# Kernel tuning notes

Hardware: AMD Instinct MI355X
Metric: run time of the kernel (lower is better)

Reference implementation:

```python
import jax, jax.numpy as jnp
import numpy as np

EPS = 1e-5

def rmsnorm(x, g):
    var = jnp.mean(jnp.square(x), axis=-1, keepdims=True)
    return x * jax.lax.rsqrt(var + EPS) * g

def setup_inputs() -> dict:
    key = jax.random.key(0)
    ks = jax.random.split(key, 8)
    B, S, T, D = 2, 2048, 2048, 1024
    H, HKV, HD = 16, 4, 64
    std = 0.02
    return {
        "x": jax.random.normal(ks[0], (B, S, D), jnp.float32),
        "kv": jax.random.normal(ks[1], (B, T, D), jnp.float32),
        "wq": jax.random.normal(ks[2], (H * HD, D), jnp.float32) * std,
        "wk": jax.random.normal(ks[3], (HKV * HD, D), jnp.float32) * std,
        "wv": jax.random.normal(ks[4], (HKV * HD, D), jnp.float32) * std,
        "wo": jax.random.normal(ks[5], (D, H * HD), jnp.float32) * std,
        "gq": jnp.ones((D,), jnp.float32),
        "gkv": jnp.ones((D,), jnp.float32),
    }

def reference(x, kv, wq, wk, wv, wo, gq, gkv):
    B, S, D = x.shape
    T = kv.shape[1]
    H, HKV, HD = 16, 4, 64
    R = H // HKV  # heads per kv group
    xn = rmsnorm(x, gq)
    kvn = rmsnorm(kv, gkv)
    # projections
    q = (xn @ wq.T).reshape(B, S, HKV, R, HD)   # grouped query heads
    k = (kvn @ wk.T).reshape(B, T, HKV, HD)
    v = (kvn @ wv.T).reshape(B, T, HKV, HD)
    scale = 1.0 / jnp.sqrt(jnp.float32(HD))
    # block-mask is None -> full dense cross attention; GQA via broadcast einsum
    scores = jnp.einsum('bsgrd,btgd->bgrst', q, k) * scale  # [B,HKV,R,S,T]
    probs = jax.nn.softmax(scores, axis=-1)
    out = jnp.einsum('bgrst,btgd->bsgrd', probs, v)  # [B,S,HKV,R,HD]
    out = out.reshape(B, S, H * HD) @ wo.T
    return x + out
```

## Files before the change

### kernel.cpp

```cpp
#include <hip/hip_runtime.h>

#define DEV __device__ __forceinline__

typedef __attribute__((ext_vector_type(8))) short frag8;
typedef __attribute__((ext_vector_type(8))) _Float16 h8;
typedef __attribute__((ext_vector_type(4))) float f32x4;

DEV unsigned short f2bf(float f) {
  union { float f; unsigned int u; } v; v.f = f;
  unsigned int r = v.u + 0x7fffu + ((v.u >> 16) & 1u);
  return (unsigned short)(r >> 16);
}

DEV unsigned short f2h(float f) {
  union { _Float16 h[2]; unsigned short u[2]; } v;
  v.h[0] = (_Float16)f;
  return v.u[0];
}

DEV float h2f(unsigned short u) {
  union { _Float16 h[2]; unsigned short u[2]; } v;
  v.u[0] = u;
  return (float)v.h[0];
}

DEV unsigned int pack2h(float a, float b) {
  union { __fp16 __attribute__((ext_vector_type(2))) p; unsigned int u; } v;
  v.p = __builtin_amdgcn_cvt_pkrtz(a, b);
  return v.u;
}

DEV void async_load16(const void* g, void* l) {
  __builtin_amdgcn_global_load_lds(
      (const __attribute__((address_space(1))) void*)g,
      (__attribute__((address_space(3))) void*)l,
      16, 0, 0);
}

__global__ __launch_bounds__(256) void fused_cast(const float* __restrict__ wq,
                                                  const float* __restrict__ wk,
                                                  const float* __restrict__ wv,
                                                  const float* __restrict__ wo,
                                                  unsigned short* __restrict__ wqb,
                                                  unsigned short* __restrict__ wkvb,
                                                  unsigned short* __restrict__ wob,
                                                  float qscale) {
  const int b = blockIdx.x;
  const float* src;
  unsigned short* dst;
  float sc = 1.0f;
  int base;
  if (b < 1024) { src = wq; dst = wqb; sc = qscale; base = b; }
  else if (b < 1280) { src = wk; dst = wkvb; base = b - 1024; }
  else if (b < 1536) { src = wv; dst = wkvb + 262144; base = b - 1280; }
  else { src = wo; dst = wob; base = b - 1536; }
  const int i = (base * 256 + threadIdx.x) * 4;
  float4 v = *(const float4*)&src[i];
  ushort4 o;
  o.x = f2bf(v.x * sc); o.y = f2bf(v.y * sc);
  o.z = f2bf(v.z * sc); o.w = f2bf(v.w * sc);
  *(ushort4*)&dst[i] = o;
}

__global__ __launch_bounds__(256) void rmsnorm2(const float* __restrict__ x,
                                                const float* __restrict__ kv,
                                                const float* __restrict__ gq,
                                                const float* __restrict__ gkv,
                                                unsigned short* __restrict__ xn,
                                                unsigned short* __restrict__ kvn) {
  int row = blockIdx.x;
  const int tid = threadIdx.x;
  const float* src;
  const float* g;
  unsigned short* dst;
  if (row < 4096) { src = x; g = gq; dst = xn; }
  else { row -= 4096; src = kv; g = gkv; dst = kvn; }
  const float* xr = src + (size_t)row * 1024;
  float4 v = *(const float4*)&xr[tid * 4];
  float ss = v.x * v.x + v.y * v.y + v.z * v.z + v.w * v.w;
  ss += __shfl_xor(ss, 32); ss += __shfl_xor(ss, 16);
  ss += __shfl_xor(ss, 8);  ss += __shfl_xor(ss, 4);
  ss += __shfl_xor(ss, 2);  ss += __shfl_xor(ss, 1);
  __shared__ float red[4];
  if ((tid & 63) == 0) red[tid >> 6] = ss;
  __syncthreads();
  float tot = red[0] + red[1] + red[2] + red[3];
  float inv = rsqrtf(tot * (1.0f / 1024.0f) + 1e-5f);
  float4 gv = *(const float4*)&g[tid * 4];
  ushort4 o;
  o.x = f2bf(v.x * inv * gv.x); o.y = f2bf(v.y * inv * gv.y);
  o.z = f2bf(v.z * inv * gv.z); o.w = f2bf(v.w * inv * gv.w);
  *(ushort4*)&dst[(size_t)row * 1024 + tid * 4] = o;
}

template <int BM, int BN, int MODE>
__global__ __launch_bounds__(256) void gemm_bt(const unsigned short* __restrict__ A,
                                               const unsigned short* __restrict__ W,
                                               void* __restrict__ out,
                                               const float* __restrict__ resid,
                                               unsigned short* __restrict__ out2,
                                               int M, int N, int K) {
  constexpr int MI = BM / 32, NI = BN / 32;
  constexpr int PA = BM / 32, PB = BN / 32;
  __shared__ unsigned short Al[2][2][BM * 32];
  __shared__ unsigned short Bl[2][2][BN * 32];
  const int tid = threadIdx.x;
  const int w = tid >> 6, l = tid & 63;
  const int quad = l >> 4, ln = l & 15;
  const int m0 = blockIdx.y * BM, n0 = blockIdx.x * BN;
  const int wm0 = (w >> 1) * (MI * 16), wn0 = (w & 1) * (NI * 16);
  const int r4 = l >> 2;
  const int c4 = (l & 3) * 8;

  f32x4 acc[MI][NI] = {};

  auto stage = [&](int buf, int kk) {
#pragma unroll
    for (int j = 0; j < PA; ++j) {
      const int idx = w * PA + j;
      const int p = idx / (BM / 16), c = idx % (BM / 16);
      async_load16(A + (size_t)(m0 + c * 16 + r4) * K + kk + p * 32 + c4,
                   &Al[buf][p][c * 512]);
    }
#pragma unroll
    for (int j = 0; j < PB; ++j) {
      const int idx = w * PB + j;
      const int p = idx / (BN / 16), c = idx % (BN / 16);
      async_load16(W + (size_t)(n0 + c * 16 + r4) * K + kk + p * 32 + c4,
                   &Bl[buf][p][c * 512]);
    }
  };

  stage(0, 0);
  const int iters = K >> 6;
#pragma unroll 2
  for (int it = 0; it < iters; ++it) {
    const int buf = it & 1;
    __syncthreads();
    if (it + 1 < iters) stage(buf ^ 1, (it + 1) << 6);
#pragma unroll
    for (int kc = 0; kc < 2; ++kc) {
      frag8 af[MI], bfr[NI];
#pragma unroll
      for (int mi = 0; mi < MI; ++mi)
        af[mi] = *(const frag8*)&Al[buf][kc][(wm0 + mi * 16 + ln) * 32 + quad * 8];
#pragma unroll
      for (int ni = 0; ni < NI; ++ni)
        bfr[ni] = *(const frag8*)&Bl[buf][kc][(wn0 + ni * 16 + ln) * 32 + quad * 8];
#pragma unroll
      for (int mi = 0; mi < MI; ++mi)
#pragma unroll
        for (int ni = 0; ni < NI; ++ni)
          acc[mi][ni] = __builtin_amdgcn_mfma_f32_16x16x32_bf16(af[mi], bfr[ni], acc[mi][ni], 0, 0, 0);
    }
  }

#pragma unroll
  for (int mi = 0; mi < MI; ++mi) {
#pragma unroll
    for (int ni = 0; ni < NI; ++ni) {
#pragma unroll
      for (int r = 0; r < 4; ++r) {
        const int row = m0 + wm0 + mi * 16 + quad * 4 + r;
        const int col = n0 + wn0 + ni * 16 + ln;
        const float v = acc[mi][ni][r];
        if (MODE == 0) {
          ((unsigned short*)out)[(size_t)row * N + col] = f2bf(v);
        } else if (MODE == 2) {
          const size_t idx = (size_t)row * N + col;
          ((float*)out)[idx] = resid[idx] + v;
        } else {
          if (col < 256) {
            ((unsigned short*)out)[(size_t)row * 256 + col] = f2bf(v);
          } else {
            const int c2 = col - 256, gg = c2 >> 6, dd = c2 & 63;
            const int bb = row >> 11, t = row & 2047;
            out2[((size_t)((bb * 4 + gg) * 64 + dd) << 11) + t] = f2h(v);
          }
        }
      }
    }
  }
}

__global__ __launch_bounds__(256, 4) void flash_attn(const unsigned short* __restrict__ q,
                                                     const unsigned short* __restrict__ k,
                                                     const unsigned short* __restrict__ vT,
                                                     unsigned short* __restrict__ o0,
                                                     unsigned short* __restrict__ o1,
                                                     float* __restrict__ l0p,
                                                     float* __restrict__ l1p) {
  __shared__ unsigned short KV[4][64 * 32];
  __shared__ unsigned short P[4 * 32 * 72];

  const int tid = threadIdx.x;
  const int w = tid >> 6, l = tid & 63;
  const int quad = l >> 4, ln = l & 15;
  const int s0 = blockIdx.x * 128;
  const int h = blockIdx.y, g = h >> 2;
  const int b = blockIdx.z >> 1, ts = blockIdx.z & 1;
  const int tbase = ts << 10;

  unsigned short* Opart = ts ? o1 : o0;
  float* lpart = ts ? l1p : l0p;

  frag8 qf[2][2];
#pragma unroll
  for (int nq = 0; nq < 2; ++nq)
#pragma unroll
    for (int c = 0; c < 2; ++c)
      qf[nq][c] = *(const frag8*)&q[(((size_t)(b * 2048 + s0 + w * 32 + nq * 16 + ln)) << 10) +
                                    h * 64 + c * 32 + quad * 8];

  f32x4 oacc[2][4] = {};
  float lsum[2] = {0.0f, 0.0f};

  const unsigned short* kbase = k + ((size_t)(b * 2048)) * 256 + g * 64;
  const unsigned short* vbase = vT + (((size_t)(b * 4 + g) * 64) << 11);
  unsigned short* Pw = &P[w * 32 * 72];

  const int r4 = l >> 2;
  const int c4 = (l & 3) * 8;

  for (int it = 0; it < 16; ++it) {
    const int t0 = tbase + it * 64;
    __syncthreads();
#pragma unroll
    for (int c = 0; c < 4; ++c) {
      const unsigned short* src;
      if (w < 2)
        src = kbase + (size_t)(t0 + c * 16 + r4) * 256 + w * 32 + c4;
      else
        src = vbase + (((size_t)(c * 16 + r4)) << 11) + t0 + (w - 2) * 32 + c4;
      async_load16(src, &KV[w][c * 512]);
    }
    __syncthreads();

    f32x4 st[2][4];
#pragma unroll
    for (int tb = 0; tb < 4; ++tb) {
      frag8 ka = *(const frag8*)&KV[0][(tb * 16 + ln) * 32 + quad * 8];
      frag8 kb2 = *(const frag8*)&KV[1][(tb * 16 + ln) * 32 + quad * 8];
#pragma unroll
      for (int nq = 0; nq < 2; ++nq) {
        f32x4 s = {};
        s = __builtin_amdgcn_mfma_f32_16x16x32_bf16(ka, qf[nq][0], s, 0, 0, 0);
        s = __builtin_amdgcn_mfma_f32_16x16x32_bf16(kb2, qf[nq][1], s, 0, 0, 0);
        st[nq][tb] = s;
      }
    }

#pragma unroll
    for (int nq = 0; nq < 2; ++nq) {
#pragma unroll
      for (int tb = 0; tb < 4; ++tb) {
        float p0 = __builtin_amdgcn_exp2f(fminf(st[nq][tb][0], 14.0f));
        float p1 = __builtin_amdgcn_exp2f(fminf(st[nq][tb][1], 14.0f));
        float p2 = __builtin_amdgcn_exp2f(fminf(st[nq][tb][2], 14.0f));
        float p3 = __builtin_amdgcn_exp2f(fminf(st[nq][tb][3], 14.0f));
        lsum[nq] += (p0 + p1) + (p2 + p3);
        uint2 pk; pk.x = pack2h(p0, p1); pk.y = pack2h(p2, p3);
        *(uint2*)&Pw[(nq * 16 + ln) * 72 + tb * 16 + quad * 4] = pk;
      }
    }

    asm volatile("s_waitcnt lgkmcnt(0)" ::: "memory");

#pragma unroll
    for (int c = 0; c < 2; ++c) {
      h8 pf0 = *(const h8*)&Pw[(0 * 16 + ln) * 72 + c * 32 + quad * 8];
      h8 pf1 = *(const h8*)&Pw[(1 * 16 + ln) * 72 + c * 32 + quad * 8];
#pragma unroll
      for (int cb = 0; cb < 4; ++cb) {
        h8 vb = *(const h8*)&KV[2 + c][(cb * 16 + ln) * 32 + quad * 8];
        oacc[0][cb] = __builtin_amdgcn_mfma_f32_16x16x32_f16(pf0, vb, oacc[0][cb], 0, 0, 0);
        oacc[1][cb] = __builtin_amdgcn_mfma_f32_16x16x32_f16(pf1, vb, oacc[1][cb], 0, 0, 0);
      }
    }
  }

#pragma unroll
  for (int nq = 0; nq < 2; ++nq) {
    lsum[nq] += __shfl_xor(lsum[nq], 16);
    lsum[nq] += __shfl_xor(lsum[nq], 32);
    if (l < 16)
      lpart[(size_t)(b * 2048 + s0 + w * 32 + nq * 16 + l) * 16 + h] = lsum[nq];
#pragma unroll
    for (int r = 0; r < 4; ++r) {
      const size_t row = (size_t)(b * 2048 + s0 + w * 32 + nq * 16 + quad * 4 + r);
#pragma unroll
      for (int cb = 0; cb < 4; ++cb)
        Opart[(row << 10) + h * 64 + cb * 16 + ln] = f2h(oacc[nq][cb][r]);
    }
  }
}

__global__ __launch_bounds__(256) void combine(const unsigned short* __restrict__ O0,
                                               const unsigned short* __restrict__ O1,
                                               const float* __restrict__ l0p,
                                               const float* __restrict__ l1p,
                                               unsigned short* __restrict__ att) {
  const int row = blockIdx.x, tid = threadIdx.x;
  const int col = tid * 4;
  const int h = tid >> 4;
  const float inv = 1.0f / (l0p[row * 16 + h] + l1p[row * 16 + h]);
  const size_t idx = ((size_t)row << 10) + col;
  ushort4 a = *(const ushort4*)&O0[idx];
  ushort4 b = *(const ushort4*)&O1[idx];
  ushort4 o;
  o.x = f2bf((h2f(a.x) + h2f(b.x)) * inv);
  o.y = f2bf((h2f(a.y) + h2f(b.y)) * inv);
  o.z = f2bf((h2f(a.z) + h2f(b.z)) * inv);
  o.w = f2bf((h2f(a.w) + h2f(b.w)) * inv);
  *(ushort4*)&att[idx] = o;
}

extern "C" void kernel_launch(void* const* d_in, const int* in_sizes, int n_in,
                              void* d_out, int out_size, void* d_ws, size_t ws_size,
                              hipStream_t stream) {
  const float* x   = (const float*)d_in[0];
  const float* kv  = (const float*)d_in[1];
  const float* wq  = (const float*)d_in[2];
  const float* wk  = (const float*)d_in[3];
  const float* wv  = (const float*)d_in[4];
  const float* wo  = (const float*)d_in[5];
  const float* gq  = (const float*)d_in[6];
  const float* gkv = (const float*)d_in[7];

  char* ws = (char*)d_ws;
  unsigned short* xn   = (unsigned short*)(ws);
  unsigned short* kvn  = (unsigned short*)(ws + 8388608);
  unsigned short* qb   = (unsigned short*)(ws + 16777216);
  unsigned short* kb   = (unsigned short*)(ws + 25165824);
  unsigned short* vTb  = (unsigned short*)(ws + 27262976);
  unsigned short* attb = (unsigned short*)(ws + 29360128);
  unsigned short* wqb  = (unsigned short*)(ws + 37748736);
  unsigned short* wkvb = (unsigned short*)(ws + 39845888);
  unsigned short* wob  = (unsigned short*)(ws + 40894464);
  unsigned short* Opart0 = xn;
  unsigned short* Opart1 = kvn;
  float* l0p = (float*)wqb;
  float* l1p = (float*)(ws + 37748736 + 262144);

  const float qscale = 0.18033688011112042f;
  fused_cast<<<2560, 256, 0, stream>>>(wq, wk, wv, wo, wqb, wkvb, wob, qscale);
  rmsnorm2<<<8192, 256, 0, stream>>>(x, kv, gq, gkv, xn, kvn);

  gemm_bt<64, 64, 0><<<dim3(16, 64), 256, 0, stream>>>(xn, wqb, qb, nullptr, nullptr,
                                                       4096, 1024, 1024);
  gemm_bt<64, 64, 3><<<dim3(8, 64), 256, 0, stream>>>(kvn, wkvb, kb, nullptr, vTb,
                                                      4096, 512, 1024);

  flash_attn<<<dim3(16, 16, 4), 256, 0, stream>>>(qb, kb, vTb, Opart0, Opart1, l0p, l1p);
  combine<<<4096, 256, 0, stream>>>(Opart0, Opart1, l0p, l1p, attb);

  gemm_bt<64, 64, 2><<<dim3(16, 64), 256, 0, stream>>>(attb, wob, d_out, x, nullptr,
                                                       4096, 1024, 1024);
}
```

Measured before the change: 204.1 us.

## Merge prep kernels and Q/KV GEMMs, switch bf16 to fp16, retile GEMMs

Fuses the weight cast and rmsnorm into one prep kernel, and the Q and KV projections into one GEMM launch. Every intermediate now uses fp16 with f16 MFMA instead of bf16. GEMM tiles grow to 128x64, but the double-buffered async prefetch is replaced by a single-buffer load-sync-compute loop. The goal is fewer launches and more reuse per tile, at the cost of losing load/compute overlap and facing fp16 range limits.

```diff
diff --git a/kernel.cpp b/kernel.cpp
--- a/kernel.cpp
+++ b/kernel.cpp
@@ -2,15 +2,8 @@
 
 #define DEV __device__ __forceinline__
 
-typedef __attribute__((ext_vector_type(8))) short frag8;
 typedef __attribute__((ext_vector_type(8))) _Float16 h8;
 typedef __attribute__((ext_vector_type(4))) float f32x4;
-
-DEV unsigned short f2bf(float f) {
-  union { float f; unsigned int u; } v; v.f = f;
-  unsigned int r = v.u + 0x7fffu + ((v.u >> 16) & 1u);
-  return (unsigned short)(r >> 16);
-}
 
 DEV unsigned short f2h(float f) {
   union { _Float16 h[2]; unsigned short u[2]; } v;
@@ -37,39 +30,39 @@
       16, 0, 0);
 }
 
-__global__ __launch_bounds__(256) void fused_cast(const float* __restrict__ wq,
-                                                  const float* __restrict__ wk,
-                                                  const float* __restrict__ wv,
-                                                  const float* __restrict__ wo,
-                                                  unsigned short* __restrict__ wqb,
-                                                  unsigned short* __restrict__ wkvb,
-                                                  unsigned short* __restrict__ wob,
-                                                  float qscale) {
-  const int b = blockIdx.x;
-  const float* src;
-  unsigned short* dst;
-  float sc = 1.0f;
-  int base;
-  if (b < 1024) { src = wq; dst = wqb; sc = qscale; base = b; }
-  else if (b < 1280) { src = wk; dst = wkvb; base = b - 1024; }
-  else if (b < 1536) { src = wv; dst = wkvb + 262144; base = b - 1280; }
-  else { src = wo; dst = wob; base = b - 1536; }
-  const int i = (base * 256 + threadIdx.x) * 4;
-  float4 v = *(const float4*)&src[i];
-  ushort4 o;
-  o.x = f2bf(v.x * sc); o.y = f2bf(v.y * sc);
-  o.z = f2bf(v.z * sc); o.w = f2bf(v.w * sc);
-  *(ushort4*)&dst[i] = o;
-}
-
-__global__ __launch_bounds__(256) void rmsnorm2(const float* __restrict__ x,
-                                                const float* __restrict__ kv,
-                                                const float* __restrict__ gq,
-                                                const float* __restrict__ gkv,
-                                                unsigned short* __restrict__ xn,
-                                                unsigned short* __restrict__ kvn) {
-  int row = blockIdx.x;
-  const int tid = threadIdx.x;
+__global__ __launch_bounds__(256) void prep(const float* __restrict__ x,
+                                            const float* __restrict__ kv,
+                                            const float* __restrict__ wq,
+                                            const float* __restrict__ wk,
+                                            const float* __restrict__ wv,
+                                            const float* __restrict__ wo,
+                                            const float* __restrict__ gq,
+                                            const float* __restrict__ gkv,
+                                            unsigned short* __restrict__ wqb,
+                                            unsigned short* __restrict__ wkvb,
+                                            unsigned short* __restrict__ wob,
+                                            unsigned short* __restrict__ xn,
+                                            unsigned short* __restrict__ kvn,
+                                            float qscale) {
+  const int b = blockIdx.x, tid = threadIdx.x;
+  if (b < 2560) {
+    const float* src;
+    unsigned short* dst;
+    float sc = 1.0f;
+    int base;
+    if (b < 1024) { src = wq; dst = wqb; sc = qscale; base = b; }
+    else if (b < 1280) { src = wk; dst = wkvb; base = b - 1024; }
+    else if (b < 1536) { src = wv; dst = wkvb + 262144; base = b - 1280; }
+    else { src = wo; dst = wob; base = b - 1536; }
+    const int i = (base * 256 + tid) * 4;
+    float4 v = *(const float4*)&src[i];
+    ushort4 o;
+    o.x = f2h(v.x * sc); o.y = f2h(v.y * sc);
+    o.z = f2h(v.z * sc); o.w = f2h(v.w * sc);
+    *(ushort4*)&dst[i] = o;
+    return;
+  }
+  int row = b - 2560;
   const float* src;
   const float* g;
   unsigned short* dst;
@@ -88,99 +81,117 @@
   float inv = rsqrtf(tot * (1.0f / 1024.0f) + 1e-5f);
   float4 gv = *(const float4*)&g[tid * 4];
   ushort4 o;
-  o.x = f2bf(v.x * inv * gv.x); o.y = f2bf(v.y * inv * gv.y);
-  o.z = f2bf(v.z * inv * gv.z); o.w = f2bf(v.w * inv * gv.w);
+  o.x = f2h(v.x * inv * gv.x); o.y = f2h(v.y * inv * gv.y);
+  o.z = f2h(v.z * inv * gv.z); o.w = f2h(v.w * inv * gv.w);
   *(ushort4*)&dst[(size_t)row * 1024 + tid * 4] = o;
 }
 
-template <int BM, int BN, int MODE>
-__global__ __launch_bounds__(256) void gemm_bt(const unsigned short* __restrict__ A,
-                                               const unsigned short* __restrict__ W,
-                                               void* __restrict__ out,
-                                               const float* __restrict__ resid,
-                                               unsigned short* __restrict__ out2,
-                                               int M, int N, int K) {
-  constexpr int MI = BM / 32, NI = BN / 32;
-  constexpr int PA = BM / 32, PB = BN / 32;
-  __shared__ unsigned short Al[2][2][BM * 32];
-  __shared__ unsigned short Bl[2][2][BN * 32];
+#define GEMM_KLOOP(A_, W_, m0_, n0_, Al_, Bl_, acc_)                                   \
+  for (int kk = 0; kk < 1024; kk += 64) {                                              \
+    __syncthreads();                                                                   \
+    _Pragma("unroll") for (int j = 0; j < 6; ++j) {                                    \
+      const int idx = w * 6 + j;                                                       \
+      if (idx < 16) {                                                                  \
+        const int p = idx >> 3, rb = (idx & 7) * 16;                                   \
+        async_load16(A_ + (size_t)(m0_ + rb + r4) * 1024 + kk + p * 32 + c4,           \
+                     &Al_[p][rb * 32]);                                                \
+      } else {                                                                         \
+        const int ib = idx - 16;                                                       \
+        const int p = ib >> 2, rb = (ib & 3) * 16;                                     \
+        async_load16(W_ + (size_t)(n0_ + rb + r4) * 1024 + kk + p * 32 + c4,           \
+                     &Bl_[p][rb * 32]);                                                \
+      }                                                                                \
+    }                                                                                  \
+    __syncthreads();                                                                   \
+    _Pragma("unroll") for (int kc = 0; kc < 2; ++kc) {                                 \
+      h8 af[4], bf[2];                                                                 \
+      _Pragma("unroll") for (int mi = 0; mi < 4; ++mi)                                 \
+        af[mi] = *(const h8*)&Al_[kc][(wm0 + mi * 16 + ln) * 32 + quad * 8];           \
+      _Pragma("unroll") for (int ni = 0; ni < 2; ++ni)                                 \
+        bf[ni] = *(const h8*)&Bl_[kc][(wn0 + ni * 16 + ln) * 32 + quad * 8];           \
+      _Pragma("unroll") for (int mi = 0; mi < 4; ++mi)                                 \
+        _Pragma("unroll") for (int ni = 0; ni < 2; ++ni)                               \
+          acc_[mi][ni] =                                                               \
+              __builtin_amdgcn_mfma_f32_16x16x32_f16(af[mi], bf[ni], acc_[mi][ni],     \
+                                                     0, 0, 0);                         \
+    }                                                                                  \
+  }
+
+__global__ __launch_bounds__(256) void proj_gemm(const unsigned short* __restrict__ xn,
+                                                 const unsigned short* __restrict__ kvn,
+                                                 const unsigned short* __restrict__ wqb,
+                                                 const unsigned short* __restrict__ wkvb,
+                                                 unsigned short* __restrict__ qb,
+                                                 unsigned short* __restrict__ kb,
+                                                 unsigned short* __restrict__ vTb) {
+  __shared__ unsigned short Al[2][128 * 32];
+  __shared__ unsigned short Bl[2][64 * 32];
   const int tid = threadIdx.x;
   const int w = tid >> 6, l = tid & 63;
   const int quad = l >> 4, ln = l & 15;
-  const int m0 = blockIdx.y * BM, n0 = blockIdx.x * BN;
-  const int wm0 = (w >> 1) * (MI * 16), wn0 = (w & 1) * (NI * 16);
+  const int wm0 = (w >> 1) * 64, wn0 = (w & 1) * 32;
   const int r4 = l >> 2;
   const int c4 = (l & 3) * 8;
 
-  f32x4 acc[MI][NI] = {};
-
-  auto stage = [&](int buf, int kk) {
-#pragma unroll
-    for (int j = 0; j < PA; ++j) {
-      const int idx = w * PA + j;
-      const int p = idx / (BM / 16), c = idx % (BM / 16);
-      async_load16(A + (size_t)(m0 + c * 16 + r4) * K + kk + p * 32 + c4,
-                   &Al[buf][p][c * 512]);
-    }
-#pragma unroll
-    for (int j = 0; j < PB; ++j) {
-      const int idx = w * PB + j;
-      const int p = idx / (BN / 16), c = idx % (BN / 16);
-      async_load16(W + (size_t)(n0 + c * 16 + r4) * K + kk + p * 32 + c4,
-                   &Bl[buf][p][c * 512]);
-    }
-  };
-
-  stage(0, 0);
-  const int iters = K >> 6;
-#pragma unroll 2
-  for (int it = 0; it < iters; ++it) {
-    const int buf = it & 1;
-    __syncthreads();
-    if (it + 1 < iters) stage(buf ^ 1, (it + 1) << 6);
-#pragma unroll
-    for (int kc = 0; kc < 2; ++kc) {
-      frag8 af[MI], bfr[NI];
-#pragma unroll
-      for (int mi = 0; mi < MI; ++mi)
-        af[mi] = *(const frag8*)&Al[buf][kc][(wm0 + mi * 16 + ln) * 32 + quad * 8];
-#pragma unroll
-      for (int ni = 0; ni < NI; ++ni)
-        bfr[ni] = *(const frag8*)&Bl[buf][kc][(wn0 + ni * 16 + ln) * 32 + quad * 8];
-#pragma unroll
-      for (int mi = 0; mi < MI; ++mi)
-#pragma unroll
-        for (int ni = 0; ni < NI; ++ni)
-          acc[mi][ni] = __builtin_amdgcn_mfma_f32_16x16x32_bf16(af[mi], bfr[ni], acc[mi][ni], 0, 0, 0);
-    }
-  }
-
-#pragma unroll
-  for (int mi = 0; mi < MI; ++mi) {
-#pragma unroll
-    for (int ni = 0; ni < NI; ++ni) {
+  int z = blockIdx.x;
+  const unsigned short *A, *W;
+  int m0, n0, isq;
+  if (z < 512) { A = xn; W = wqb; m0 = (z >> 4) * 128; n0 = (z & 15) * 64; isq = 1; }
+  else { z -= 512; A = kvn; W = wkvb; m0 = (z >> 3) * 128; n0 = (z & 7) * 64; isq = 0; }
+
+  f32x4 acc[4][2] = {};
+  GEMM_KLOOP(A, W, m0, n0, Al, Bl, acc)
+
+#pragma unroll
+  for (int mi = 0; mi < 4; ++mi)
+#pragma unroll
+    for (int ni = 0; ni < 2; ++ni)
 #pragma unroll
       for (int r = 0; r < 4; ++r) {
         const int row = m0 + wm0 + mi * 16 + quad * 4 + r;
         const int col = n0 + wn0 + ni * 16 + ln;
-        const float v = acc[mi][ni][r];
-        if (MODE == 0) {
-          ((unsigned short*)out)[(size_t)row * N + col] = f2bf(v);
-        } else if (MODE == 2) {
-          const size_t idx = (size_t)row * N + col;
-          ((float*)out)[idx] = resid[idx] + v;
+        const unsigned short v = f2h(acc[mi][ni][r]);
+        if (isq) {
+          qb[((size_t)row << 10) + col] = v;
+        } else if (col < 256) {
+          kb[(size_t)row * 256 + col] = v;
         } else {
-          if (col < 256) {
-            ((unsigned short*)out)[(size_t)row * 256 + col] = f2bf(v);
-          } else {
-            const int c2 = col - 256, gg = c2 >> 6, dd = c2 & 63;
-            const int bb = row >> 11, t = row & 2047;
-            out2[((size_t)((bb * 4 + gg) * 64 + dd) << 11) + t] = f2h(v);
-          }
+          const int c2 = col - 256, gg = c2 >> 6, dd = c2 & 63;
+          const int bb = row >> 11, t = row & 2047;
+          vTb[((size_t)((bb * 4 + gg) * 64 + dd) << 11) + t] = v;
         }
       }
-    }
-  }
+}
+
+__global__ __launch_bounds__(256) void o_gemm(const unsigned short* __restrict__ attb,
+                                              const unsigned short* __restrict__ wob,
+                                              const float* __restrict__ x,
+                                              float* __restrict__ out) {
+  __shared__ unsigned short Al[2][128 * 32];
+  __shared__ unsigned short Bl[2][64 * 32];
+  const int tid = threadIdx.x;
+  const int w = tid >> 6, l = tid & 63;
+  const int quad = l >> 4, ln = l & 15;
+  const int wm0 = (w >> 1) * 64, wn0 = (w & 1) * 32;
+  const int r4 = l >> 2;
+  const int c4 = (l & 3) * 8;
+
+  const int m0 = (blockIdx.x >> 4) * 128, n0 = (blockIdx.x & 15) * 64;
+
+  f32x4 acc[4][2] = {};
+  GEMM_KLOOP(attb, wob, m0, n0, Al, Bl, acc)
+
+#pragma unroll
+  for (int mi = 0; mi < 4; ++mi)
+#pragma unroll
+    for (int ni = 0; ni < 2; ++ni)
+#pragma unroll
+      for (int r = 0; r < 4; ++r) {
+        const int row = m0 + wm0 + mi * 16 + quad * 4 + r;
+        const int col = n0 + wn0 + ni * 16 + ln;
+        const size_t idx = ((size_t)row << 10) + col;
+        out[idx] = x[idx] + acc[mi][ni][r];
+      }
 }
 
 __global__ __launch_bounds__(256, 4) void flash_attn(const unsigned short* __restrict__ q,
@@ -204,13 +215,13 @@
   unsigned short* Opart = ts ? o1 : o0;
   float* lpart = ts ? l1p : l0p;
 
-  frag8 qf[2][2];
+  h8 qf[2][2];
 #pragma unroll
   for (int nq = 0; nq < 2; ++nq)
 #pragma unroll
     for (int c = 0; c < 2; ++c)
-      qf[nq][c] = *(const frag8*)&q[(((size_t)(b * 2048 + s0 + w * 32 + nq * 16 + ln)) << 10) +
-                                    h * 64 + c * 32 + quad * 8];
+      qf[nq][c] = *(const h8*)&q[(((size_t)(b * 2048 + s0 + w * 32 + nq * 16 + ln)) << 10) +
+                                 h * 64 + c * 32 + quad * 8];
 
   f32x4 oacc[2][4] = {};
   float lsum[2] = {0.0f, 0.0f};
@@ -239,13 +250,13 @@
     f32x4 st[2][4];
 #pragma unroll
     for (int tb = 0; tb < 4; ++tb) {
-      frag8 ka = *(const frag8*)&KV[0][(tb * 16 + ln) * 32 + quad * 8];
-      frag8 kb2 = *(const frag8*)&KV[1][(tb * 16 + ln) * 32 + quad * 8];
+      h8 ka = *(const h8*)&KV[0][(tb * 16 + ln) * 32 + quad * 8];
+      h8 kb2 = *(const h8*)&KV[1][(tb * 16 + ln) * 32 + quad * 8];
 #pragma unroll
       for (int nq = 0; nq < 2; ++nq) {
         f32x4 s = {};
-        s = __builtin_amdgcn_mfma_f32_16x16x32_bf16(ka, qf[nq][0], s, 0, 0, 0);
-        s = __builtin_amdgcn_mfma_f32_16x16x32_bf16(kb2, qf[nq][1], s, 0, 0, 0);
+        s = __builtin_amdgcn_mfma_f32_16x16x32_f16(ka, qf[nq][0], s, 0, 0, 0);
+        s = __builtin_amdgcn_mfma_f32_16x16x32_f16(kb2, qf[nq][1], s, 0, 0, 0);
         st[nq][tb] = s;
       }
     }
@@ -308,10 +319,10 @@
   ushort4 a = *(const ushort4*)&O0[idx];
   ushort4 b = *(const ushort4*)&O1[idx];
   ushort4 o;
-  o.x = f2bf((h2f(a.x) + h2f(b.x)) * inv);
-  o.y = f2bf((h2f(a.y) + h2f(b.y)) * inv);
-  o.z = f2bf((h2f(a.z) + h2f(b.z)) * inv);
-  o.w = f2bf((h2f(a.w) + h2f(b.w)) * inv);
+  o.x = f2h((h2f(a.x) + h2f(b.x)) * inv);
+  o.y = f2h((h2f(a.y) + h2f(b.y)) * inv);
+  o.z = f2h((h2f(a.z) + h2f(b.z)) * inv);
+  o.w = f2h((h2f(a.w) + h2f(b.w)) * inv);
   *(ushort4*)&att[idx] = o;
 }
 
@@ -343,17 +354,14 @@
   float* l1p = (float*)(ws + 37748736 + 262144);
 
   const float qscale = 0.18033688011112042f;
-  fused_cast<<<2560, 256, 0, stream>>>(wq, wk, wv, wo, wqb, wkvb, wob, qscale);
-  rmsnorm2<<<8192, 256, 0, stream>>>(x, kv, gq, gkv, xn, kvn);
-
-  gemm_bt<64, 64, 0><<<dim3(16, 64), 256, 0, stream>>>(xn, wqb, qb, nullptr, nullptr,
-                                                       4096, 1024, 1024);
-  gemm_bt<64, 64, 3><<<dim3(8, 64), 256, 0, stream>>>(kvn, wkvb, kb, nullptr, vTb,
-                                                      4096, 512, 1024);
+
+  prep<<<10752, 256, 0, stream>>>(x, kv, wq, wk, wv, wo, gq, gkv,
+                                  wqb, wkvb, wob, xn, kvn, qscale);
+
+  proj_gemm<<<768, 256, 0, stream>>>(xn, kvn, wqb, wkvb, qb, kb, vTb);
 
   flash_attn<<<dim3(16, 16, 4), 256, 0, stream>>>(qb, kb, vTb, Opart0, Opart1, l0p, l1p);
   combine<<<4096, 256, 0, stream>>>(Opart0, Opart1, l0p, l1p, attb);
 
-  gemm_bt<64, 64, 2><<<dim3(16, 64), 256, 0, stream>>>(attb, wob, d_out, x, nullptr,
-                                                       4096, 1024, 1024);
-}
+  o_gemm<<<512, 256, 0, stream>>>(attb, wob, x, (float*)d_out);
+}
```

Result: no change. 200.9 us (-1.6%).
